# Optimization experiments

Hardware: AMD Instinct MI355X
Metric: run time of the kernel (lower is better)

Reference implementation:

```python
import jax, jax.numpy as jnp
import numpy as np

B, C_IMG, H, W = 16, 512, 32, 32
C_AUD, K_LEN, N_HEADS = 512, 256, 8
HEAD_DIM = C_AUD // N_HEADS
EPS = 1e-5


def setup_inputs() -> dict:
    key = jax.random.key(0)
    ks = jax.random.split(key, 12)
    s_img = 1.0 / np.sqrt(C_IMG)
    s_aud = 1.0 / np.sqrt(C_AUD)
    return {
        "img_feat": jax.random.normal(ks[0], (B, C_IMG, H, W), jnp.float32),
        "audio_feat": jax.random.normal(ks[1], (B, K_LEN, C_AUD), jnp.float32),
        "Wq": jax.random.uniform(ks[2], (C_IMG, C_AUD), jnp.float32, -s_img, s_img),
        "bq": jnp.zeros((C_AUD,), jnp.float32),
        "Wk": jax.random.uniform(ks[3], (C_AUD, C_AUD), jnp.float32, -s_aud, s_aud),
        "bk": jnp.zeros((C_AUD,), jnp.float32),
        "Wv": jax.random.uniform(ks[4], (C_AUD, C_AUD), jnp.float32, -s_aud, s_aud),
        "bv": jnp.zeros((C_AUD,), jnp.float32),
        "Wo": jax.random.uniform(ks[5], (C_AUD, C_IMG), jnp.float32, -s_aud, s_aud),
        "bo": jnp.zeros((C_IMG,), jnp.float32),
        "gamma": jnp.ones((C_IMG,), jnp.float32),
        "beta": jnp.zeros((C_IMG,), jnp.float32),
    }


def reference(img_feat, audio_feat, Wq, bq, Wk, bk, Wv, bv, Wo, bo, gamma, beta):
    b, c, h, w = img_feat.shape
    # b c h w -> b (h w) c
    img_seq = img_feat.reshape(b, c, h * w).transpose(0, 2, 1)
    q = img_seq @ Wq + bq                      # [b, q, C_AUD]
    k = audio_feat @ Wk + bk                   # [b, k, C_AUD]
    v = audio_feat @ Wv + bv
    # split heads: b s (h d) -> b h s d
    def split(x):
        bs, s, _ = x.shape
        return x.reshape(bs, s, N_HEADS, HEAD_DIM).transpose(0, 2, 1, 3)
    qh, kh, vh = split(q), split(k), split(v)
    scale = HEAD_DIM ** -0.5
    scores = jnp.einsum('bhqd,bhkd->bhqk', qh, kh) * scale
    weights = jax.nn.softmax(scores, axis=-1)
    attn = jnp.einsum('bhqk,bhkd->bhqd', weights, vh)
    attn = attn.transpose(0, 2, 1, 3).reshape(b, h * w, C_AUD)
    proj = attn @ Wo + bo                      # [b, q, C_IMG]
    y = img_seq + proj
    mu = jnp.mean(y, axis=-1, keepdims=True)
    var = jnp.mean((y - mu) ** 2, axis=-1, keepdims=True)
    y = (y - mu) * jax.lax.rsqrt(var + EPS) * gamma + beta
    # b (h w) c -> b c h w
    return y.transpose(0, 2, 1).reshape(b, c, h, w)
```

## Files before the change

kernel.cpp:

```cpp
#include <hip/hip_runtime.h>
#include <cstddef>

#define B_SZ 16
#define HW 1024
#define CCH 512
#define K_LEN 256
#define N_HEADS 8
#define EPS 1e-5f

typedef __bf16 bf16;
typedef bf16 bf16x8 __attribute__((ext_vector_type(8)));
typedef bf16 bf16x4 __attribute__((ext_vector_type(4)));
typedef float f32x4 __attribute__((ext_vector_type(4)));

__device__ __forceinline__ void gl_lds16(const bf16* g, bf16* l) {
    __builtin_amdgcn_global_load_lds(
        (const __attribute__((address_space(1))) void*)g,
        (__attribute__((address_space(3))) void*)l, 16, 0, 0);
}

__global__ __launch_bounds__(256) void prep_kernel(
    const float* __restrict__ img, const float* __restrict__ audio,
    const float* __restrict__ Wq, const float* __restrict__ Wk,
    const float* __restrict__ Wv, const float* __restrict__ Wo,
    bf16* __restrict__ img_bf, bf16* __restrict__ aud_bf, bf16* __restrict__ wT)
{
    __shared__ bf16 T[64][72];
    const int bid = blockIdx.x;
    const int tid = threadIdx.x;

    if (bid < 2048) {
        const int s0 = (bid & 15) * 64;
        const int c0 = ((bid >> 4) & 7) * 64;
        const int b  = bid >> 7;
        {
            const int r = tid >> 2, cs = (tid & 3) << 4;
            const float* sp = img + ((size_t)b * CCH + c0 + r) * HW + s0 + cs;
            #pragma unroll
            for (int i = 0; i < 4; ++i) {
                float4 f = *(const float4*)(sp + i * 4);
                T[r][cs + i*4 + 0] = (bf16)f.x;
                T[r][cs + i*4 + 1] = (bf16)f.y;
                T[r][cs + i*4 + 2] = (bf16)f.z;
                T[r][cs + i*4 + 3] = (bf16)f.w;
            }
        }
        __syncthreads();
        {
            const int ss = tid >> 2, ks = (tid & 3) << 4;
            bf16x8 a, b8;
            #pragma unroll
            for (int j = 0; j < 8; ++j) { a[j] = T[ks + j][ss]; b8[j] = T[ks + 8 + j][ss]; }
            bf16* dp = img_bf + ((size_t)b * HW + s0 + ss) * CCH + c0 + ks;
            *(bf16x8*)dp = a;
            *(bf16x8*)(dp + 8) = b8;
        }
    } else if (bid < 3072) {
        const size_t i = ((size_t)(bid - 2048) * 256 + tid) * 8;
        float4 a = *(const float4*)(audio + i);
        float4 b = *(const float4*)(audio + i + 4);
        bf16x8 o;
        o[0] = (bf16)a.x; o[1] = (bf16)a.y; o[2] = (bf16)a.z; o[3] = (bf16)a.w;
        o[4] = (bf16)b.x; o[5] = (bf16)b.y; o[6] = (bf16)b.z; o[7] = (bf16)b.w;
        *(bf16x8*)(aud_bf + i) = o;
    } else {
        const int b2 = bid - 3072;
        const int n0 = (b2 & 7) * 64;
        const int k0 = ((b2 >> 3) & 7) * 64;
        const int w  = b2 >> 6;
        const float* src = (w == 0) ? Wq : (w == 1) ? Wk : (w == 2) ? Wv : Wo;
        {
            const int r = tid >> 2, cs = (tid & 3) << 4;
            const float* sp = src + (size_t)(k0 + r) * CCH + n0 + cs;
            #pragma unroll
            for (int i = 0; i < 4; ++i) {
                float4 f = *(const float4*)(sp + i * 4);
                T[r][cs + i*4 + 0] = (bf16)f.x;
                T[r][cs + i*4 + 1] = (bf16)f.y;
                T[r][cs + i*4 + 2] = (bf16)f.z;
                T[r][cs + i*4 + 3] = (bf16)f.w;
            }
        }
        __syncthreads();
        {
            const int nn = tid >> 2, ks = (tid & 3) << 4;
            bf16x8 a, b8;
            #pragma unroll
            for (int j = 0; j < 8; ++j) { a[j] = T[ks + j][nn]; b8[j] = T[ks + 8 + j][nn]; }
            bf16* dp = wT + (size_t)w * CCH * CCH + (size_t)(n0 + nn) * CCH + k0 + ks;
            *(bf16x8*)dp = a;
            *(bf16x8*)(dp + 8) = b8;
        }
    }
}

__global__ __launch_bounds__(256) void gemm_bf16_mfma(
    const bf16* __restrict__ A, const bf16* __restrict__ Bt,
    const float* __restrict__ bias, bf16* __restrict__ out)
{
    const int bid  = blockIdx.x;
    const int g    = bid >> 5, rr = bid & 31;
    const int m0 = (g * 8 + (rr & 7)) * 128;
    const int n0 = (rr >> 3) * 128;
    const int tid  = threadIdx.x;
    const int wave = tid >> 6, lane = tid & 63;
    const int l15 = lane & 15, quad = lane >> 4;
    const int wm = (wave >> 1) * 64, wn = (wave & 1) * 64;

    __shared__ bf16 As[128 * 32];
    __shared__ bf16 Bs[128 * 32];

    const int r16 = lane >> 2;
    const int ks  = (lane & 3) * 8;

    f32x4 acc[4][4];
    #pragma unroll
    for (int i = 0; i < 4; ++i)
        #pragma unroll
        for (int j = 0; j < 4; ++j)
            acc[i][j] = (f32x4){0.f, 0.f, 0.f, 0.f};

    for (int k0 = 0; k0 < 512; k0 += 32) {
        #pragma unroll
        for (int i = 0; i < 2; ++i) {
            const int c = wave * 2 + i;
            gl_lds16(A  + (size_t)(m0 + c * 16 + r16) * 512 + k0 + ks, &As[c * 512]);
            gl_lds16(Bt + (size_t)(n0 + c * 16 + r16) * 512 + k0 + ks, &Bs[c * 512]);
        }
        __syncthreads();
        bf16x8 af[4], bfr[4];
        #pragma unroll
        for (int i = 0; i < 4; ++i)
            af[i] = *(const bf16x8*)&As[(wm + i * 16 + l15) * 32 + quad * 8];
        #pragma unroll
        for (int j = 0; j < 4; ++j)
            bfr[j] = *(const bf16x8*)&Bs[(wn + j * 16 + l15) * 32 + quad * 8];
        #pragma unroll
        for (int i = 0; i < 4; ++i)
            #pragma unroll
            for (int j = 0; j < 4; ++j)
                acc[i][j] = __builtin_amdgcn_mfma_f32_16x16x32_bf16(bfr[j], af[i], acc[i][j], 0, 0, 0);
        __syncthreads();
    }

    #pragma unroll
    for (int j = 0; j < 4; ++j) {
        const int gn = n0 + wn + j * 16 + quad * 4;
        const float4 bv4 = *(const float4*)(bias + gn);
        const float bb[4] = {bv4.x, bv4.y, bv4.z, bv4.w};
        #pragma unroll
        for (int i = 0; i < 4; ++i) {
            const int gm = m0 + wm + i * 16 + l15;
            bf16x4 ov;
            #pragma unroll
            for (int r = 0; r < 4; ++r) ov[r] = (bf16)(acc[i][j][r] + bb[r]);
            *(bf16x4*)(out + (size_t)gm * 512 + gn) = ov;
        }
    }
}

__global__ __launch_bounds__(256) void qkv_gemm(
    const bf16* __restrict__ imgA, const bf16* __restrict__ WqT,
    const float* __restrict__ bq, bf16* __restrict__ qout,
    const bf16* __restrict__ audA, const bf16* __restrict__ WkvT,
    const float* __restrict__ bk, const float* __restrict__ bv,
    bf16* __restrict__ khout, bf16* __restrict__ vtout)
{
    const int bid  = blockIdx.x;
    const int tid  = threadIdx.x;
    const int wave = tid >> 6, lane = tid & 63;
    const int l15 = lane & 15, quad = lane >> 4;
    const int wm = (wave >> 1) * 64, wn = (wave & 1) * 64;

    __shared__ bf16 As[128 * 32];
    __shared__ bf16 Bs[128 * 32];

    const int r16 = lane >> 2;
    const int ks  = (lane & 3) * 8;

    f32x4 acc[4][4];
    #pragma unroll
    for (int i = 0; i < 4; ++i)
        #pragma unroll
        for (int j = 0; j < 4; ++j)
            acc[i][j] = (f32x4){0.f, 0.f, 0.f, 0.f};

    if (bid < 512) {
        const int g = bid >> 5, rr = bid & 31;
        const int m0 = (g * 8 + (rr & 7)) * 128;
        const int n0 = (rr >> 3) * 128;

        for (int k0 = 0; k0 < 512; k0 += 32) {
            #pragma unroll
            for (int i = 0; i < 2; ++i) {
                const int c = wave * 2 + i;
                gl_lds16(imgA + (size_t)(m0 + c * 16 + r16) * 512 + k0 + ks, &As[c * 512]);
                gl_lds16(WqT  + (size_t)(n0 + c * 16 + r16) * 512 + k0 + ks, &Bs[c * 512]);
            }
            __syncthreads();
            bf16x8 af[4], bfr[4];
            #pragma unroll
            for (int i = 0; i < 4; ++i)
                af[i] = *(const bf16x8*)&As[(wm + i * 16 + l15) * 32 + quad * 8];
            #pragma unroll
            for (int j = 0; j < 4; ++j)
                bfr[j] = *(const bf16x8*)&Bs[(wn + j * 16 + l15) * 32 + quad * 8];
            #pragma unroll
            for (int i = 0; i < 4; ++i)
                #pragma unroll
                for (int j = 0; j < 4; ++j)
                    acc[i][j] = __builtin_amdgcn_mfma_f32_16x16x32_bf16(bfr[j], af[i], acc[i][j], 0, 0, 0);
            __syncthreads();
        }

        #pragma unroll
        for (int j = 0; j < 4; ++j) {
            const int gn = n0 + wn + j * 16 + quad * 4;
            const float4 bv4 = *(const float4*)(bq + gn);
            const float bb[4] = {bv4.x, bv4.y, bv4.z, bv4.w};
            #pragma unroll
            for (int i = 0; i < 4; ++i) {
                const int gm = m0 + wm + i * 16 + l15;
                bf16x4 ov;
                #pragma unroll
                for (int r = 0; r < 4; ++r) ov[r] = (bf16)(acc[i][j][r] + bb[r]);
                *(bf16x4*)(qout + (size_t)gm * 512 + gn) = ov;
            }
        }
    } else {
        const int b2 = bid - 512;
        const int g = b2 >> 6, rr = b2 & 63;
        const int m0 = (g * 8 + (rr & 7)) * 128;
        const int n0 = (rr >> 3) * 128;

        for (int k0 = 0; k0 < 512; k0 += 32) {
            #pragma unroll
            for (int i = 0; i < 2; ++i) {
                const int c = wave * 2 + i;
                gl_lds16(audA + (size_t)(m0 + c * 16 + r16) * 512 + k0 + ks, &As[c * 512]);
                gl_lds16(WkvT + (size_t)(n0 + c * 16 + r16) * 512 + k0 + ks, &Bs[c * 512]);
            }
            __syncthreads();
            bf16x8 af[4], bfr[4];
            #pragma unroll
            for (int i = 0; i < 4; ++i)
                af[i] = *(const bf16x8*)&As[(wm + i * 16 + l15) * 32 + quad * 8];
            #pragma unroll
            for (int j = 0; j < 4; ++j)
                bfr[j] = *(const bf16x8*)&Bs[(wn + j * 16 + l15) * 32 + quad * 8];
            #pragma unroll
            for (int i = 0; i < 4; ++i)
                #pragma unroll
                for (int j = 0; j < 4; ++j)
                    acc[i][j] = __builtin_amdgcn_mfma_f32_16x16x32_bf16(af[i], bfr[j], acc[i][j], 0, 0, 0);
            __syncthreads();
        }

        #pragma unroll
        for (int j = 0; j < 4; ++j) {
            const int gn = n0 + wn + j * 16 + l15;
            if (gn < 512) {
                const int h = gn >> 6, d = gn & 63;
                const float bias = bk[gn];
                #pragma unroll
                for (int i = 0; i < 4; ++i) {
                    const int gm = m0 + wm + i * 16 + quad * 4;
                    const int b = gm >> 8, key = gm & 255;
                    bf16* base = khout + ((((size_t)b * N_HEADS + h) * K_LEN) + key) * 64 + d;
                    #pragma unroll
                    for (int r = 0; r < 4; ++r)
                        base[(size_t)r * 64] = (bf16)(acc[i][j][r] + bias);
                }
            } else {
                const int ch = gn - 512;
                const int h = ch >> 6, d = ch & 63;
                const float bias = bv[ch];
                #pragma unroll
                for (int i = 0; i < 4; ++i) {
                    const int gm = m0 + wm + i * 16 + quad * 4;
                    const int b = gm >> 8, key = gm & 255;
                    bf16x4 pk;
                    #pragma unroll
                    for (int r = 0; r < 4; ++r) pk[r] = (bf16)(acc[i][j][r] + bias);
                    *(bf16x4*)(vtout + (((size_t)b * N_HEADS + h) * 64 + d) * K_LEN + key) = pk;
                }
            }
        }
    }
}

__global__ __launch_bounds__(256) void attn_mfma(
    const bf16* __restrict__ q,
    const bf16* __restrict__ kh,
    const bf16* __restrict__ vt,
    bf16* __restrict__ o)
{
    const int bid = blockIdx.x;
    const int xcd = bid & 7, idx = bid >> 3;
    const int bh  = xcd + 8 * (idx >> 4);
    const int s0  = (idx & 15) * 64;
    const int tid = threadIdx.x;
    const int wave = tid >> 6, lane = tid & 63;
    const int l15 = lane & 15, quad = lane >> 4;
    const int b = bh >> 3, h = bh & 7;

    __shared__ bf16 KsPt[18432];
    __shared__ bf16 Vs[16896];

    const bf16* khb = kh + (size_t)bh * K_LEN * 64;
    const bf16* vtb = vt + (size_t)bh * 64 * K_LEN;

    #pragma unroll
    for (int i = 0; i < 8; ++i) {
        const int chunk = tid + (i << 8);
        const int key = chunk >> 3, dseg = (chunk & 7) << 3;
        *(bf16x8*)&KsPt[key * 72 + dseg] = *(const bf16x8*)(khb + key * 64 + dseg);
        const int d = chunk >> 5, kseg = (chunk & 31) << 3;
        *(bf16x8*)&Vs[d * 264 + kseg] = *(const bf16x8*)(vtb + d * 256 + kseg);
    }
    __syncthreads();

    const int qrow = s0 + wave * 16 + l15;
    const bf16* qp = q + ((size_t)(b * HW + qrow)) * 512 + h * 64 + quad * 8;
    const bf16x8 qf0 = *(const bf16x8*)qp;
    const bf16x8 qf1 = *(const bf16x8*)(qp + 32);

    f32x4 acc[16];
    #pragma unroll
    for (int m = 0; m < 16; ++m) acc[m] = (f32x4){0.f, 0.f, 0.f, 0.f};
    __builtin_amdgcn_s_setprio(1);
    #pragma unroll
    for (int m = 0; m < 16; ++m) {
        const bf16x8 a0 = *(const bf16x8*)&KsPt[(m * 16 + l15) * 72 + quad * 8];
        const bf16x8 a1 = *(const bf16x8*)&KsPt[(m * 16 + l15) * 72 + 32 + quad * 8];
        acc[m] = __builtin_amdgcn_mfma_f32_16x16x32_bf16(a0, qf0, acc[m], 0, 0, 0);
        acc[m] = __builtin_amdgcn_mfma_f32_16x16x32_bf16(a1, qf1, acc[m], 0, 0, 0);
    }
    __builtin_amdgcn_s_setprio(0);

    float mx = -1e30f;
    #pragma unroll
    for (int m = 0; m < 16; ++m)
        mx = fmaxf(mx, fmaxf(fmaxf(acc[m][0], acc[m][1]), fmaxf(acc[m][2], acc[m][3])));
    mx = fmaxf(mx, __shfl_xor(mx, 16, 64));
    mx = fmaxf(mx, __shfl_xor(mx, 32, 64));

    __syncthreads();

    bf16* PtW = &KsPt[wave * 4224];
    float l_sum = 0.f;
    #pragma unroll
    for (int m = 0; m < 16; ++m) {
        bf16x4 pk;
        #pragma unroll
        for (int r = 0; r < 4; ++r) {
            const float p = __expf((acc[m][r] - mx) * 0.125f);
            l_sum += p;
            pk[r] = (bf16)p;
        }
        *(bf16x4*)&PtW[l15 * 264 + m * 16 + quad * 4] = pk;
    }
    l_sum += __shfl_xor(l_sum, 16, 64);
    l_sum += __shfl_xor(l_sum, 32, 64);

    f32x4 oacc[4];
    #pragma unroll
    for (int m = 0; m < 4; ++m) oacc[m] = (f32x4){0.f, 0.f, 0.f, 0.f};
    __builtin_amdgcn_s_setprio(1);
    #pragma unroll
    for (int s = 0; s < 8; ++s) {
        const bf16x8 pb = *(const bf16x8*)&PtW[l15 * 264 + s * 32 + quad * 8];
        #pragma unroll
        for (int m = 0; m < 4; ++m) {
            const bf16x8 va = *(const bf16x8*)&Vs[(m * 16 + l15) * 264 + s * 32 + quad * 8];
            oacc[m] = __builtin_amdgcn_mfma_f32_16x16x32_bf16(va, pb, oacc[m], 0, 0, 0);
        }
    }
    __builtin_amdgcn_s_setprio(0);

    const float inv = 1.0f / l_sum;
    bf16* op = o + ((size_t)(b * HW + qrow)) * 512 + h * 64 + quad * 4;
    #pragma unroll
    for (int m = 0; m < 4; ++m) {
        bf16x4 ov;
        #pragma unroll
        for (int r = 0; r < 4; ++r) ov[r] = (bf16)(oacc[m][r] * inv);
        *(bf16x4*)&op[m * 16] = ov;
    }
}

__global__ __launch_bounds__(256) void ln_kernel(
    const bf16* __restrict__ proj, const bf16* __restrict__ imgb,
    const float* __restrict__ gamma, const float* __restrict__ beta,
    float* __restrict__ out)
{
    const int b  = blockIdx.y;
    const int s0 = blockIdx.x * 32;
    const int tid = threadIdx.x;
    const int wave = tid >> 6, lane = tid & 63;

    __shared__ float Y[32][513];

    const int cb = lane * 8;
    const float4 g0 = *(const float4*)(gamma + cb);
    const float4 g1 = *(const float4*)(gamma + cb + 4);
    const float4 b0 = *(const float4*)(beta + cb);
    const float4 b1 = *(const float4*)(beta + cb + 4);
    const float gg[8] = {g0.x, g0.y, g0.z, g0.w, g1.x, g1.y, g1.z, g1.w};
    const float bb[8] = {b0.x, b0.y, b0.z, b0.w, b1.x, b1.y, b1.z, b1.w};

    #pragma unroll
    for (int rr = 0; rr < 8; ++rr) {
        const int ss = wave * 8 + rr;
        const size_t row = (size_t)b * HW + s0 + ss;
        bf16x8 p8 = *(const bf16x8*)(proj + row * 512 + cb);
        bf16x8 i8 = *(const bf16x8*)(imgb + row * 512 + cb);
        float y[8];
        float sum = 0.f, sq = 0.f;
        #pragma unroll
        for (int j = 0; j < 8; ++j) {
            y[j] = (float)p8[j] + (float)i8[j];
            sum += y[j]; sq += y[j] * y[j];
        }
        #pragma unroll
        for (int off = 32; off > 0; off >>= 1) {
            sum += __shfl_xor(sum, off, 64);
            sq  += __shfl_xor(sq, off, 64);
        }
        const float mu = sum * (1.f / 512.f);
        const float rs = rsqrtf(sq * (1.f / 512.f) - mu * mu + EPS);
        #pragma unroll
        for (int j = 0; j < 8; ++j)
            Y[ss][cb + j] = (y[j] - mu) * rs * gg[j] + bb[j];
    }
    __syncthreads();

    #pragma unroll
    for (int it = 0; it < 16; ++it) {
        const int idx = it * 256 + tid;
        const int c = idx >> 3, sseg = (idx & 7) << 2;
        float4 o4;
        o4.x = Y[sseg + 0][c];
        o4.y = Y[sseg + 1][c];
        o4.z = Y[sseg + 2][c];
        o4.w = Y[sseg + 3][c];
        *(float4*)(out + ((size_t)b * CCH + c) * HW + s0 + sseg) = o4;
    }
}

extern "C" void kernel_launch(void* const* d_in, const int* in_sizes, int n_in,
                              void* d_out, int out_size, void* d_ws, size_t ws_size,
                              hipStream_t stream) {
    const float* img   = (const float*)d_in[0];
    const float* audio = (const float*)d_in[1];
    const float* Wq    = (const float*)d_in[2];
    const float* bq    = (const float*)d_in[3];
    const float* Wk    = (const float*)d_in[4];
    const float* bk    = (const float*)d_in[5];
    const float* Wv    = (const float*)d_in[6];
    const float* bv    = (const float*)d_in[7];
    const float* Wo    = (const float*)d_in[8];
    const float* bo    = (const float*)d_in[9];
    const float* gamma = (const float*)d_in[10];
    const float* beta  = (const float*)d_in[11];

    bf16* wsb    = (bf16*)d_ws;
    bf16* img_bf = wsb;
    bf16* aud_bf = img_bf + 8388608;
    bf16* wT     = aud_bf + 2097152;
    bf16* q_bf   = wT + 1048576;
    bf16* kh_bf  = q_bf + 8388608;
    bf16* vt_bf  = kh_bf + 2097152;
    bf16* a_bf   = vt_bf + 2097152;
    bf16* p_bf   = q_bf;

    prep_kernel<<<dim3(3328), 256, 0, stream>>>(img, audio, Wq, Wk, Wv, Wo,
                                                img_bf, aud_bf, wT);
    qkv_gemm<<<dim3(768), 256, 0, stream>>>(img_bf, wT, bq, q_bf,
                                            aud_bf, wT + 262144, bk, bv, kh_bf, vt_bf);
    attn_mfma<<<dim3(B_SZ * N_HEADS * (HW / 64)), 256, 0, stream>>>(q_bf, kh_bf, vt_bf, a_bf);
    gemm_bf16_mfma<<<dim3(512), 256, 0, stream>>>(a_bf, wT + 3 * 262144, bo, p_bf);
    ln_kernel<<<dim3(32, 16), 256, 0, stream>>>(p_bf, img_bf, gamma, beta, (float*)d_out);
}
```

Before: 185.7 us.

## Double-buffer LDS tiles in GEMM kernels with async prefetch two steps ahead

The shared-memory A/B tiles in the output-projection GEMM and the fused QKV GEMM become two-stage ping-pong buffers. Global-to-LDS loads for step t+2 are issued right after step t's compute, and explicit vmcnt waits plus raw barriers replace the old __syncthreads pair. The goal is to overlap global memory latency with MFMA work instead of stalling on every K step. This doubles LDS per block, which may lower occupancy, and relies on hand-written waitcnt counts being correct.

```diff
diff --git a/kernel.cpp b/kernel.cpp
--- a/kernel.cpp
+++ b/kernel.cpp
@@ -107,11 +107,16 @@
     const int l15 = lane & 15, quad = lane >> 4;
     const int wm = (wave >> 1) * 64, wn = (wave & 1) * 64;
 
-    __shared__ bf16 As[128 * 32];
-    __shared__ bf16 Bs[128 * 32];
+    __shared__ bf16 As[2][128 * 32];
+    __shared__ bf16 Bs[2][128 * 32];
 
     const int r16 = lane >> 2;
     const int ks  = (lane & 3) * 8;
+    const int c0c = wave * 2, c1c = wave * 2 + 1;
+    const bf16* a0p = A  + (size_t)(m0 + c0c * 16 + r16) * 512 + ks;
+    const bf16* a1p = A  + (size_t)(m0 + c1c * 16 + r16) * 512 + ks;
+    const bf16* b0p = Bt + (size_t)(n0 + c0c * 16 + r16) * 512 + ks;
+    const bf16* b1p = Bt + (size_t)(n0 + c1c * 16 + r16) * 512 + ks;
 
     f32x4 acc[4][4];
     #pragma unroll
@@ -120,27 +125,34 @@
         for (int j = 0; j < 4; ++j)
             acc[i][j] = (f32x4){0.f, 0.f, 0.f, 0.f};
 
-    for (int k0 = 0; k0 < 512; k0 += 32) {
-        #pragma unroll
-        for (int i = 0; i < 2; ++i) {
-            const int c = wave * 2 + i;
-            gl_lds16(A  + (size_t)(m0 + c * 16 + r16) * 512 + k0 + ks, &As[c * 512]);
-            gl_lds16(Bt + (size_t)(n0 + c * 16 + r16) * 512 + k0 + ks, &Bs[c * 512]);
-        }
-        __syncthreads();
+    gl_lds16(a0p,      &As[0][c0c * 512]); gl_lds16(a1p,      &As[0][c1c * 512]);
+    gl_lds16(b0p,      &Bs[0][c0c * 512]); gl_lds16(b1p,      &Bs[0][c1c * 512]);
+    gl_lds16(a0p + 32, &As[1][c0c * 512]); gl_lds16(a1p + 32, &As[1][c1c * 512]);
+    gl_lds16(b0p + 32, &Bs[1][c0c * 512]); gl_lds16(b1p + 32, &Bs[1][c1c * 512]);
+
+    for (int t = 0; t < 16; ++t) {
+        if (t < 15) asm volatile("s_waitcnt vmcnt(4)" ::: "memory");
+        else        asm volatile("s_waitcnt vmcnt(0)" ::: "memory");
+        __builtin_amdgcn_s_barrier();
+        const int cur = t & 1;
         bf16x8 af[4], bfr[4];
         #pragma unroll
         for (int i = 0; i < 4; ++i)
-            af[i] = *(const bf16x8*)&As[(wm + i * 16 + l15) * 32 + quad * 8];
+            af[i] = *(const bf16x8*)&As[cur][(wm + i * 16 + l15) * 32 + quad * 8];
         #pragma unroll
         for (int j = 0; j < 4; ++j)
-            bfr[j] = *(const bf16x8*)&Bs[(wn + j * 16 + l15) * 32 + quad * 8];
+            bfr[j] = *(const bf16x8*)&Bs[cur][(wn + j * 16 + l15) * 32 + quad * 8];
         #pragma unroll
         for (int i = 0; i < 4; ++i)
             #pragma unroll
             for (int j = 0; j < 4; ++j)
                 acc[i][j] = __builtin_amdgcn_mfma_f32_16x16x32_bf16(bfr[j], af[i], acc[i][j], 0, 0, 0);
-        __syncthreads();
+        __builtin_amdgcn_s_barrier();
+        if (t < 14) {
+            const int ko = (t + 2) * 32;
+            gl_lds16(a0p + ko, &As[cur][c0c * 512]); gl_lds16(a1p + ko, &As[cur][c1c * 512]);
+            gl_lds16(b0p + ko, &Bs[cur][c0c * 512]); gl_lds16(b1p + ko, &Bs[cur][c1c * 512]);
+        }
     }
 
     #pragma unroll
@@ -172,11 +184,12 @@
     const int l15 = lane & 15, quad = lane >> 4;
     const int wm = (wave >> 1) * 64, wn = (wave & 1) * 64;
 
-    __shared__ bf16 As[128 * 32];
-    __shared__ bf16 Bs[128 * 32];
+    __shared__ bf16 As[2][128 * 32];
+    __shared__ bf16 Bs[2][128 * 32];
 
     const int r16 = lane >> 2;
     const int ks  = (lane & 3) * 8;
+    const int c0c = wave * 2, c1c = wave * 2 + 1;
 
     f32x4 acc[4][4];
     #pragma unroll
@@ -189,28 +202,39 @@
         const int g = bid >> 5, rr = bid & 31;
         const int m0 = (g * 8 + (rr & 7)) * 128;
         const int n0 = (rr >> 3) * 128;
-
-        for (int k0 = 0; k0 < 512; k0 += 32) {
-            #pragma unroll
-            for (int i = 0; i < 2; ++i) {
-                const int c = wave * 2 + i;
-                gl_lds16(imgA + (size_t)(m0 + c * 16 + r16) * 512 + k0 + ks, &As[c * 512]);
-                gl_lds16(WqT  + (size_t)(n0 + c * 16 + r16) * 512 + k0 + ks, &Bs[c * 512]);
-            }
-            __syncthreads();
+        const bf16* a0p = imgA + (size_t)(m0 + c0c * 16 + r16) * 512 + ks;
+        const bf16* a1p = imgA + (size_t)(m0 + c1c * 16 + r16) * 512 + ks;
+        const bf16* b0p = WqT  + (size_t)(n0 + c0c * 16 + r16) * 512 + ks;
+        const bf16* b1p = WqT  + (size_t)(n0 + c1c * 16 + r16) * 512 + ks;
+
+        gl_lds16(a0p,      &As[0][c0c * 512]); gl_lds16(a1p,      &As[0][c1c * 512]);
+        gl_lds16(b0p,      &Bs[0][c0c * 512]); gl_lds16(b1p,      &Bs[0][c1c * 512]);
+        gl_lds16(a0p + 32, &As[1][c0c * 512]); gl_lds16(a1p + 32, &As[1][c1c * 512]);
+        gl_lds16(b0p + 32, &Bs[1][c0c * 512]); gl_lds16(b1p + 32, &Bs[1][c1c * 512]);
+
+        for (int t = 0; t < 16; ++t) {
+            if (t < 15) asm volatile("s_waitcnt vmcnt(4)" ::: "memory");
+            else        asm volatile("s_waitcnt vmcnt(0)" ::: "memory");
+            __builtin_amdgcn_s_barrier();
+            const int cur = t & 1;
             bf16x8 af[4], bfr[4];
             #pragma unroll
             for (int i = 0; i < 4; ++i)
-                af[i] = *(const bf16x8*)&As[(wm + i * 16 + l15) * 32 + quad * 8];
+                af[i] = *(const bf16x8*)&As[cur][(wm + i * 16 + l15) * 32 + quad * 8];
             #pragma unroll
             for (int j = 0; j < 4; ++j)
-                bfr[j] = *(const bf16x8*)&Bs[(wn + j * 16 + l15) * 32 + quad * 8];
+                bfr[j] = *(const bf16x8*)&Bs[cur][(wn + j * 16 + l15) * 32 + quad * 8];
             #pragma unroll
             for (int i = 0; i < 4; ++i)
                 #pragma unroll
                 for (int j = 0; j < 4; ++j)
                     acc[i][j] = __builtin_amdgcn_mfma_f32_16x16x32_bf16(bfr[j], af[i], acc[i][j], 0, 0, 0);
-            __syncthreads();
+            __builtin_amdgcn_s_barrier();
+            if (t < 14) {
+                const int ko = (t + 2) * 32;
+                gl_lds16(a0p + ko, &As[cur][c0c * 512]); gl_lds16(a1p + ko, &As[cur][c1c * 512]);
+                gl_lds16(b0p + ko, &Bs[cur][c0c * 512]); gl_lds16(b1p + ko, &Bs[cur][c1c * 512]);
+            }
         }
 
         #pragma unroll
@@ -232,28 +256,39 @@
         const int g = b2 >> 6, rr = b2 & 63;
         const int m0 = (g * 8 + (rr & 7)) * 128;
         const int n0 = (rr >> 3) * 128;
-
-        for (int k0 = 0; k0 < 512; k0 += 32) {
-            #pragma unroll
-            for (int i = 0; i < 2; ++i) {
-                const int c = wave * 2 + i;
-                gl_lds16(audA + (size_t)(m0 + c * 16 + r16) * 512 + k0 + ks, &As[c * 512]);
-                gl_lds16(WkvT + (size_t)(n0 + c * 16 + r16) * 512 + k0 + ks, &Bs[c * 512]);
-            }
-            __syncthreads();
+        const bf16* a0p = audA + (size_t)(m0 + c0c * 16 + r16) * 512 + ks;
+        const bf16* a1p = audA + (size_t)(m0 + c1c * 16 + r16) * 512 + ks;
+        const bf16* b0p = WkvT + (size_t)(n0 + c0c * 16 + r16) * 512 + ks;
+        const bf16* b1p = WkvT + (size_t)(n0 + c1c * 16 + r16) * 512 + ks;
+
+        gl_lds16(a0p,      &As[0][c0c * 512]); gl_lds16(a1p,      &As[0][c1c * 512]);
+        gl_lds16(b0p,      &Bs[0][c0c * 512]); gl_lds16(b1p,      &Bs[0][c1c * 512]);
+        gl_lds16(a0p + 32, &As[1][c0c * 512]); gl_lds16(a1p + 32, &As[1][c1c * 512]);
+        gl_lds16(b0p + 32, &Bs[1][c0c * 512]); gl_lds16(b1p + 32, &Bs[1][c1c * 512]);
+
+        for (int t = 0; t < 16; ++t) {
+            if (t < 15) asm volatile("s_waitcnt vmcnt(4)" ::: "memory");
+            else        asm volatile("s_waitcnt vmcnt(0)" ::: "memory");
+            __builtin_amdgcn_s_barrier();
+            const int cur = t & 1;
             bf16x8 af[4], bfr[4];
             #pragma unroll
             for (int i = 0; i < 4; ++i)
-                af[i] = *(const bf16x8*)&As[(wm + i * 16 + l15) * 32 + quad * 8];
+                af[i] = *(const bf16x8*)&As[cur][(wm + i * 16 + l15) * 32 + quad * 8];
             #pragma unroll
             for (int j = 0; j < 4; ++j)
-                bfr[j] = *(const bf16x8*)&Bs[(wn + j * 16 + l15) * 32 + quad * 8];
+                bfr[j] = *(const bf16x8*)&Bs[cur][(wn + j * 16 + l15) * 32 + quad * 8];
             #pragma unroll
             for (int i = 0; i < 4; ++i)
                 #pragma unroll
                 for (int j = 0; j < 4; ++j)
                     acc[i][j] = __builtin_amdgcn_mfma_f32_16x16x32_bf16(af[i], bfr[j], acc[i][j], 0, 0, 0);
-            __syncthreads();
+            __builtin_amdgcn_s_barrier();
+            if (t < 14) {
+                const int ko = (t + 2) * 32;
+                gl_lds16(a0p + ko, &As[cur][c0c * 512]); gl_lds16(a1p + ko, &As[cur][c1c * 512]);
+                gl_lds16(b0p + ko, &Bs[cur][c0c * 512]); gl_lds16(b1p + ko, &Bs[cur][c1c * 512]);
+            }
         }
 
         #pragma unroll
```

Result: no change. 185.1 us (-0.3%).
